# Performance work log

Hardware: AMD Instinct MI355X
Metric: run time of the kernel (lower is better)

## Reference

```python
import jax, jax.numpy as jnp
import numpy as np
import math


def setup_inputs() -> dict:
    rng = jax.random.key(0)
    k1, k2, k3 = jax.random.split(rng, 3)
    B, L, H, E = 2, 1024, 8, 64
    query = jax.random.normal(k1, (B, L, H, E), dtype=jnp.float32)
    key = jax.random.normal(k2, (B, L, H, E), dtype=jnp.float32)
    value = jax.random.normal(k3, (B, L, H, E), dtype=jnp.float32)
    mask_miss_k = jnp.zeros((B, L), dtype=bool)
    mask_miss_q = jnp.zeros((B, L), dtype=bool)
    pos = jnp.arange(B * L).reshape(B, L)
    causal_mask = 0  # unused by the module body
    # learned scalar parameters (nn.Parameter init values)
    log_gain_gate = jnp.float32(math.log(2.0))
    log_tau_gate = jnp.float32(math.log(0.5))
    log_gain_dir = jnp.float32(math.log(3.0))
    log_tau_dir = jnp.float32(math.log(0.3))
    return {
        "query": query, "key": key, "value": value,
        "mask_miss_k": mask_miss_k, "mask_miss_q": mask_miss_q,
        "pos": pos, "causal_mask": causal_mask,
        "log_gain_gate": log_gain_gate, "log_tau_gate": log_tau_gate,
        "log_gain_dir": log_gain_dir, "log_tau_dir": log_tau_dir,
    }


def reference(query, key, value, mask_miss_k, mask_miss_q, pos, causal_mask,
              log_gain_gate, log_tau_gate, log_gain_dir, log_tau_dir):
    # Multihead path: query (B,L,H,E). Eval mode, dropout p=0, dag_mask=None.
    B, L, H, E = query.shape
    scale = 1.0 / jnp.sqrt(jnp.float32(E))
    # scores: (B,H,L,S) with S == L
    scores = scale * jnp.einsum('blhe,bshe->bhls', query, key)
    scores_t = jnp.swapaxes(scores, -1, -2)
    S_sym = 0.5 * (scores + scores_t)       # symmetric part
    A_anti = 0.5 * (scores - scores_t)      # antisymmetric (Lie) part

    MAX_GAIN = 20.0
    gain_gate = jnp.clip(jnp.exp(log_gain_gate), 1e-3, MAX_GAIN)
    tau_gate = jnp.clip(jnp.exp(log_tau_gate), 1e-3, 10.0)
    gain_dir = jnp.clip(jnp.exp(log_gain_dir), 1e-3, MAX_GAIN)
    tau_dir = jnp.clip(jnp.exp(log_tau_dir), 1e-3, 10.0)

    gamma_att = gain_gate * jnp.tanh(S_sym / tau_gate)
    phi_att = gain_dir * jnp.tanh(A_anti / tau_dir)

    gate_probs = jax.nn.sigmoid(gamma_att)
    dir_probs = jax.nn.sigmoid(phi_att)
    dag_probs = gate_probs * dir_probs

    diag = jnp.eye(L, L, dtype=bool)  # P(i->i) = 0
    dag_probs = jnp.where(diag[None, None], 0.0, dag_probs)
    M = dag_probs  # eval branch; diagonal already zeroed (second fill is a no-op)

    att = jax.nn.relu(jnp.tanh(A_anti * gain_dir / tau_dir)) * M

    # entropy per query position (B,H,L)
    entropy = -jnp.sum(att * jnp.log(jnp.clip(att, 1e-8, None)), axis=-1)
    entropy = jnp.nan_to_num(entropy)

    # dropout p=0 -> identity; nan_to_num is a no-op on finite att
    V = jnp.einsum('bhls,bshd->blhd', att, value)  # (B,L,H,E)
    return V, att, entropy
```

## Files before the change

kernel.cpp:

```cpp
#include <hip/hip_runtime.h>
#include <math.h>

namespace {

typedef __bf16 bf16_t;
typedef bf16_t bf16x8 __attribute__((ext_vector_type(8)));
typedef bf16_t bf16x4 __attribute__((ext_vector_type(4)));
typedef bf16_t bf16x2 __attribute__((ext_vector_type(2)));
typedef float f32x4 __attribute__((ext_vector_type(4)));

constexpr int L = 1024;
constexpr int H = 8;
constexpr int E = 64;
constexpr int HE = H * E;
constexpr int BH = 16;
constexpr size_t PL = (size_t)BH * L * E;
constexpr float LOG2E = 1.4426950408889634f;
constexpr float LN2 = 0.6931471805599453f;

__device__ __forceinline__ float rcp_fast(float x) { return __builtin_amdgcn_rcpf(x); }
__device__ __forceinline__ float exp2_fast(float x) { return __builtin_amdgcn_exp2f(x); }
__device__ __forceinline__ float log2_fast(float x) { return __builtin_amdgcn_logf(x); }
__device__ __forceinline__ f32x4 mfma16(bf16x8 a, bf16x8 b, f32x4 c) {
  return __builtin_amdgcn_mfma_f32_16x16x32_bf16(a, b, c, 0, 0, 0);
}
__device__ __forceinline__ void split4(float4 x, bf16x4& hv, bf16x4& lv) {
  hv[0] = (bf16_t)x.x; lv[0] = (bf16_t)(x.x - (float)hv[0]);
  hv[1] = (bf16_t)x.y; lv[1] = (bf16_t)(x.y - (float)hv[1]);
  hv[2] = (bf16_t)x.z; lv[2] = (bf16_t)(x.z - (float)hv[2]);
  hv[3] = (bf16_t)x.w; lv[3] = (bf16_t)(x.w - (float)hv[3]);
}

__global__ __launch_bounds__(256) void k_prep(
    const float* __restrict__ q, const float* __restrict__ k,
    const float* __restrict__ v, bf16_t* __restrict__ ws,
    float* __restrict__ entr)
{
  const int bid = blockIdx.x;
  if (bid >= 256) {
    const int idx = (bid - 256) * 256 + threadIdx.x;
    *(float4*)(entr + (size_t)idx * 4) = make_float4(0.f, 0.f, 0.f, 0.f);
    return;
  }
  bf16_t* Qh = ws;
  bf16_t* Ql = ws + PL;
  bf16_t* Kh = ws + 2 * PL;
  bf16_t* Kl = ws + 3 * PL;
  bf16_t* VT = ws + 4 * PL;
  const int bh = bid >> 4, chunk = bid & 15;
  const int b = bh >> 3, h = bh & 7;
  const int tid = threadIdx.x, t8 = tid >> 4, c4 = tid & 15;
  __shared__ bf16_t Vb[64][72];

#pragma unroll
  for (int pass = 0; pass < 4; ++pass) {
    const int row = chunk * 64 + pass * 16 + t8;
    const size_t gin = ((size_t)(b * L + row) * H + h) * E + c4 * 4;
    const size_t gout = ((size_t)bh * L + row) * E + c4 * 4;
    float4 q4 = *(const float4*)(q + gin);
    float4 k4 = *(const float4*)(k + gin);
    float4 v4 = *(const float4*)(v + gin);
    bf16x4 hv, lv;
    split4(q4, hv, lv);
    *(bf16x4*)(Qh + gout) = hv; *(bf16x4*)(Ql + gout) = lv;
    split4(k4, hv, lv);
    *(bf16x4*)(Kh + gout) = hv; *(bf16x4*)(Kl + gout) = lv;
    const int sl = pass * 16 + t8;
    Vb[c4 * 4 + 0][sl] = (bf16_t)v4.x;
    Vb[c4 * 4 + 1][sl] = (bf16_t)v4.y;
    Vb[c4 * 4 + 2][sl] = (bf16_t)v4.z;
    Vb[c4 * 4 + 3][sl] = (bf16_t)v4.w;
  }
  __syncthreads();
#pragma unroll
  for (int pass = 0; pass < 2; ++pass) {
    const int idx = pass * 256 + tid;
    const int e = idx >> 3, ch = idx & 7;
    bf16x8 val = *(const bf16x8*)&Vb[e][ch * 8];
    *(bf16x8*)(VT + ((size_t)bh * E + e) * L + chunk * 64 + ch * 8) = val;
  }
}

__global__ __launch_bounds__(256, 2) void k_sym(
    const bf16_t* __restrict__ ws, float* __restrict__ attg,
    float* __restrict__ entr,
    const float* __restrict__ p_lgg, const float* __restrict__ p_ltg,
    const float* __restrict__ p_lgd, const float* __restrict__ p_ltd)
{
  const bf16_t* Qh = ws;
  const bf16_t* Ql = ws + PL;
  const bf16_t* Kh = ws + 2 * PL;
  const bf16_t* Kl = ws + 3 * PL;

  __shared__ __align__(16) bf16_t P_s[4][32][72];
  __shared__ __align__(16) float att2f[32][36];

  const int tid = threadIdx.x;
  const int w = tid >> 6, lane = tid & 63;
  const int c = lane & 15, qd = lane >> 4;
  const int lh = w & 1, sh = w >> 1;
  const int I = blockIdx.x, bh = blockIdx.y, z = blockIdx.z;
  const int niter = (I < 16) ? 17 : 16;
  const int itlo = z ? 8 : 0;
  const int ithi = z ? niter : 8;

  const float gg = fminf(fmaxf(__expf(p_lgg[0]), 1e-3f), 20.0f);
  const float tg = fminf(fmaxf(__expf(p_ltg[0]), 1e-3f), 10.0f);
  const float gd = fminf(fmaxf(__expf(p_lgd[0]), 1e-3f), 20.0f);
  const float td = fminf(fmaxf(__expf(p_ltd[0]), 1e-3f), 10.0f);
  const float A1 = 0.125f * (1.0f / tg) * LOG2E;
  const float A2 = 0.125f * (1.0f / td) * LOG2E;
  const float A3 = 0.125f * gd * (1.0f / td) * LOG2E;
  const float G1 = -gg * LOG2E, G1m2 = -2.0f * G1;
  const float G2 = -gd * LOG2E, G2m2 = -2.0f * G2;

  bf16x8 qaf[2][2], kaf[2][2];
  {
    const size_t aro = ((size_t)bh * L + I * 32 + lh * 16 + c) * E;
#pragma unroll
    for (int ks = 0; ks < 2; ++ks) {
      qaf[ks][0] = *(const bf16x8*)(Qh + aro + ks * 32 + qd * 8);
      qaf[ks][1] = *(const bf16x8*)(Ql + aro + ks * 32 + qd * 8);
      kaf[ks][0] = *(const bf16x8*)(Kh + aro + ks * 32 + qd * 8);
      kaf[ks][1] = *(const bf16x8*)(Kl + aro + ks * 32 + qd * 8);
    }
  }

  const bf16_t* planep = (w == 0) ? Kh : (w == 1) ? Kl : (w == 2) ? Qh : Ql;
  const int prow = lane >> 1;
  const int pcol = (lane & 1) * 32;

  bf16x8 pf0, pf1, pf2, pf3;
  {
    const size_t off =
        ((size_t)bh * L + (size_t)((I + itlo) & 31) * 32 + prow) * E + pcol;
    pf0 = *(const bf16x8*)(planep + off);
    pf1 = *(const bf16x8*)(planep + off + 8);
    pf2 = *(const bf16x8*)(planep + off + 16);
    pf3 = *(const bf16x8*)(planep + off + 24);
  }

  float entL[4] = {0.f, 0.f, 0.f, 0.f};

  for (int it = itlo; it < ithi; ++it) {
    const int J = (I + it) & 31;
    const int Jn = (I + it + 1) & 31;

    __syncthreads();
    *(bf16x8*)&P_s[w][prow][pcol]      = pf0;
    *(bf16x8*)&P_s[w][prow][pcol + 8]  = pf1;
    *(bf16x8*)&P_s[w][prow][pcol + 16] = pf2;
    *(bf16x8*)&P_s[w][prow][pcol + 24] = pf3;
    __syncthreads();

    {
      const size_t off = ((size_t)bh * L + (size_t)Jn * 32 + prow) * E + pcol;
      pf0 = *(const bf16x8*)(planep + off);
      pf1 = *(const bf16x8*)(planep + off + 8);
      pf2 = *(const bf16x8*)(planep + off + 16);
      pf3 = *(const bf16x8*)(planep + off + 24);
    }

    f32x4 acc1 = {}, acc2 = {};
    const int brow = sh * 16 + c;
#pragma unroll
    for (int ks = 0; ks < 2; ++ks) {
      bf16x8 kbh = *(const bf16x8*)&P_s[0][brow][ks * 32 + qd * 8];
      bf16x8 kbl = *(const bf16x8*)&P_s[1][brow][ks * 32 + qd * 8];
      bf16x8 qbh = *(const bf16x8*)&P_s[2][brow][ks * 32 + qd * 8];
      bf16x8 qbl = *(const bf16x8*)&P_s[3][brow][ks * 32 + qd * 8];
      acc1 = mfma16(qaf[ks][0], kbh, acc1);
      acc1 = mfma16(qaf[ks][0], kbl, acc1);
      acc1 = mfma16(qaf[ks][1], kbh, acc1);
      acc2 = mfma16(kaf[ks][0], qbh, acc2);
      acc2 = mfma16(kaf[ks][1], qbh, acc2);
      acc2 = mfma16(kaf[ks][0], qbl, acc2);
    }

    float entS = 0.f;
    float* arow = attg + ((size_t)bh * L + I * 32 + lh * 16 + qd * 4) * L +
                  (size_t)J * 32 + sh * 16;
    f32x4 a2v;
#pragma unroll
    for (int r = 0; r < 4; ++r) {
      const float u = acc1[r] + acc2[r];
      const float d = acc1[r] - acc2[r];
      const float r1 = rcp_fast(exp2_fast(u * A1) + 1.f);
      const float gate = rcp_fast(1.f + exp2_fast(fmaf(r1, G1m2, G1)));
      const float r2 = rcp_fast(exp2_fast(d * A2) + 1.f);
      const float dir = rcp_fast(1.f + exp2_fast(fmaf(r2, G2m2, G2)));
      const float t = fmaf(rcp_fast(exp2_fast(d * A3) + 1.f), -2.f, 1.f);
      const float gdp = gate * dir;
      const float a1 = fmaxf(t, 0.f) * gdp;
      const float a2 = fmaxf(-t, 0.f) * (gate - gdp);
      const float la = log2_fast(fmaxf(a1 + a2, 1e-8f));
      entL[r] -= a1 * la;
      entS -= a2 * la;
      arow[(size_t)r * L + c] = a1;
      a2v[r] = a2;
    }
    *(f32x4*)&att2f[sh * 16 + c][lh * 16 + qd * 4] = a2v;
    __syncthreads();

    if (it != 0) {
      const int mr = tid >> 3, mc = (tid & 7) * 4;
      float* orow =
          attg + ((size_t)bh * L + (size_t)J * 32 + mr) * L + (size_t)I * 32 + mc;
      *(f32x4*)orow = *(const f32x4*)&att2f[mr][mc];

      float e = entS;
      e += __shfl_xor(e, 16);
      e += __shfl_xor(e, 32);
      if (lane < 16)
        atomicAdd(entr + (size_t)bh * L + (size_t)J * 32 + sh * 16 + c, e * LN2);
    }
  }

#pragma unroll
  for (int r = 0; r < 4; ++r) {
    float e = entL[r];
    e += __shfl_xor(e, 1);
    e += __shfl_xor(e, 2);
    e += __shfl_xor(e, 4);
    e += __shfl_xor(e, 8);
    if (c == 0)
      atomicAdd(entr + (size_t)bh * L + I * 32 + lh * 16 + qd * 4 + r, e * LN2);
  }
}

__global__ __launch_bounds__(256, 2) void k_pv(
    const bf16_t* __restrict__ ws, const float* __restrict__ attg,
    float* __restrict__ Vout)
{
  const bf16_t* VT = ws + 4 * PL;
  __shared__ __align__(16) bf16_t att_s[32][72];

  const int tid = threadIdx.x;
  const int w = tid >> 6, lane = tid & 63;
  const int c = lane & 15, qd = lane >> 4;
  const int mh = w & 1, eh = w >> 1;
  const int lt = blockIdx.x, bh = blockIdx.y;
  const int b = bh >> 3, h = bh & 7;
  const int l0 = lt * 32;

  const int srow = tid >> 3, scol = (tid & 7) * 8;
  const float* abase = attg + ((size_t)bh * L + l0 + srow) * L + scol;

  f32x4 pa = *(const f32x4*)(abase);
  f32x4 pb = *(const f32x4*)(abase + 4);

  const bf16_t* vbase = VT + ((size_t)bh * E + eh * 32) * L;

  f32x4 acc[2] = {};
  for (int st = 0; st < 16; ++st) {
    __syncthreads();
    {
      bf16x8 af;
      af[0] = (bf16_t)pa[0]; af[1] = (bf16_t)pa[1];
      af[2] = (bf16_t)pa[2]; af[3] = (bf16_t)pa[3];
      af[4] = (bf16_t)pb[0]; af[5] = (bf16_t)pb[1];
      af[6] = (bf16_t)pb[2]; af[7] = (bf16_t)pb[3];
      *(bf16x8*)&att_s[srow][scol] = af;
    }
    __syncthreads();
    {
      const int stn = (st + 1) & 15;
      pa = *(const f32x4*)(abase + stn * 64);
      pb = *(const f32x4*)(abase + stn * 64 + 4);
    }
#pragma unroll
    for (int ks = 0; ks < 2; ++ks) {
      bf16x8 av = *(const bf16x8*)&att_s[mh * 16 + c][ks * 32 + qd * 8];
#pragma unroll
      for (int n = 0; n < 2; ++n) {
        bf16x8 bv = *(const bf16x8*)(vbase + (size_t)(n * 16 + c) * L +
                                     st * 64 + ks * 32 + qd * 8);
        acc[n] = mfma16(av, bv, acc[n]);
      }
    }
  }
#pragma unroll
  for (int n = 0; n < 2; ++n)
#pragma unroll
    for (int r = 0; r < 4; ++r)
      Vout[((size_t)(b * L + l0 + mh * 16 + qd * 4 + r) * H + h) * E +
           eh * 32 + n * 16 + c] = acc[n][r];
}

__device__ __forceinline__ float tanh_fast(float x) {
  return 1.0f - 2.0f * rcp_fast(__expf(2.0f * x) + 1.0f);
}
__device__ __forceinline__ float sigm_fast(float x) {
  return rcp_fast(1.0f + __expf(-x));
}
__device__ __forceinline__ void split_store(bf16_t* hi, bf16_t* lo, float4 x) {
  bf16x4 hv, lv;
  split4(x, hv, lv);
  *(bf16x4*)hi = hv;
  *(bf16x4*)lo = lv;
}

__global__ __launch_bounds__(128, 1) void fused_attn(
    const float* __restrict__ q, const float* __restrict__ kk,
    const float* __restrict__ v,
    float* __restrict__ Vout, float* __restrict__ attg, float* __restrict__ entr,
    const float* __restrict__ p_lgg, const float* __restrict__ p_ltg,
    const float* __restrict__ p_lgd, const float* __restrict__ p_ltd)
{
  constexpr int TM = 32;
  __shared__ bf16_t Qa_hi[TM][72], Qa_lo[TM][72];
  __shared__ bf16_t Ka_hi[TM][72], Ka_lo[TM][72];
  __shared__ bf16_t KQ_hi[64][72], KQ_lo[64][72];
  __shared__ bf16_t Vts[64][72];
  __shared__ float  T2ex[2][64][17];
  __shared__ bf16_t attLs[2][16][72];

  const int tid = threadIdx.x;
  const int w = tid >> 6;
  const int lane = tid & 63;
  const int c = lane & 15;
  const int qd = lane >> 4;
  const int t8 = tid >> 4;
  const int c4 = tid & 15;
  const int lt = blockIdx.x;
  const int bh = blockIdx.y;
  const int b = bh >> 3, h = bh & 7;
  const int l0 = lt * TM;

  const float gg = fminf(fmaxf(__expf(p_lgg[0]), 1e-3f), 20.0f);
  const float tg = fminf(fmaxf(__expf(p_ltg[0]), 1e-3f), 10.0f);
  const float gd = fminf(fmaxf(__expf(p_lgd[0]), 1e-3f), 20.0f);
  const float td = fminf(fmaxf(__expf(p_ltd[0]), 1e-3f), 10.0f);
  const float inv_tg = 1.0f / tg;
  const float inv_td = 1.0f / td;
  const float gd_inv_td = gd * inv_td;

  const float* qlbase = q  + ((size_t)(b * L + l0) * H + h) * E;
  const float* qsbase = q  + ((size_t)b * L * H + h) * E;
  const float* kbase  = kk + ((size_t)b * L * H + h) * E;
  const float* vbase  = v  + ((size_t)b * L * H + h) * E;

#pragma unroll
  for (int i = 0; i < 4; ++i) {
    int r = t8 + 8 * i;
    float4 qa = *(const float4*)(qlbase + (size_t)r * HE + c4 * 4);
    float4 ka = *(const float4*)(kbase + (size_t)(l0 + r) * HE + c4 * 4);
    split_store(&Qa_hi[r][c4 * 4], &Qa_lo[r][c4 * 4], qa);
    split_store(&Ka_hi[r][c4 * 4], &Ka_lo[r][c4 * 4], ka);
  }

  float4 kpre[8], qpre[8];
  float vpre[32];
#pragma unroll
  for (int i = 0; i < 8; ++i)
    kpre[i] = *(const float4*)(kbase + (size_t)(t8 + 8 * i) * HE + c4 * 4);
#pragma unroll
  for (int i = 0; i < 8; ++i)
    qpre[i] = *(const float4*)(qsbase + (size_t)(t8 + 8 * i) * HE + c4 * 4);
#pragma unroll
  for (int j = 0; j < 32; ++j)
    vpre[j] = vbase[(size_t)(w * 32 + j) * HE + lane];

  __syncthreads();

  bf16x8 qaf[2][2], kaf[2][2];
#pragma unroll
  for (int ks = 0; ks < 2; ++ks) {
    qaf[ks][0] = *(const bf16x8*)&Qa_hi[w * 16 + c][ks * 32 + qd * 8];
    qaf[ks][1] = *(const bf16x8*)&Qa_lo[w * 16 + c][ks * 32 + qd * 8];
    kaf[ks][0] = *(const bf16x8*)&Ka_hi[w * 16 + c][ks * 32 + qd * 8];
    kaf[ks][1] = *(const bf16x8*)&Ka_lo[w * 16 + c][ks * 32 + qd * 8];
  }

  f32x4 accv[4] = {};
  float ent[4] = {0.f, 0.f, 0.f, 0.f};
  const int gl_base = l0 + w * 16 + qd * 4;

  for (int it = 0; it < 16; ++it) {
    const int s0 = it * 64;
    const int snext = ((it + 1) & 15) * 64;

    __syncthreads();
#pragma unroll
    for (int i = 0; i < 8; ++i) {
      int r = t8 + 8 * i;
      split_store(&KQ_hi[r][c4 * 4], &KQ_lo[r][c4 * 4], kpre[i]);
    }
#pragma unroll
    for (int j = 0; j < 16; ++j) {
      bf16x2 p;
      p[0] = (bf16_t)vpre[2 * j];
      p[1] = (bf16_t)vpre[2 * j + 1];
      *(bf16x2*)&Vts[lane][w * 32 + 2 * j] = p;
    }
    __syncthreads();

#pragma unroll
    for (int i = 0; i < 8; ++i)
      kpre[i] = *(const float4*)(kbase + (size_t)(snext + t8 + 8 * i) * HE + c4 * 4);
#pragma unroll
    for (int j = 0; j < 32; ++j)
      vpre[j] = vbase[(size_t)(snext + w * 32 + j) * HE + lane];

    f32x4 acc1[4] = {};
#pragma unroll
    for (int nt = 0; nt < 4; ++nt) {
#pragma unroll
      for (int ks = 0; ks < 2; ++ks) {
        bf16x8 bhv = *(const bf16x8*)&KQ_hi[nt * 16 + c][ks * 32 + qd * 8];
        bf16x8 blv = *(const bf16x8*)&KQ_lo[nt * 16 + c][ks * 32 + qd * 8];
        acc1[nt] = mfma16(qaf[ks][0], bhv, acc1[nt]);
        acc1[nt] = mfma16(qaf[ks][0], blv, acc1[nt]);
        acc1[nt] = mfma16(qaf[ks][1], bhv, acc1[nt]);
      }
    }
    __syncthreads();

#pragma unroll
    for (int i = 0; i < 8; ++i) {
      int r = t8 + 8 * i;
      split_store(&KQ_hi[r][c4 * 4], &KQ_lo[r][c4 * 4], qpre[i]);
    }
    __syncthreads();

#pragma unroll
    for (int i = 0; i < 8; ++i)
      qpre[i] = *(const float4*)(qsbase + (size_t)(snext + t8 + 8 * i) * HE + c4 * 4);

    f32x4 acc2[4] = {};
#pragma unroll
    for (int mt = 0; mt < 4; ++mt) {
#pragma unroll
      for (int ks = 0; ks < 2; ++ks) {
        bf16x8 ahv = *(const bf16x8*)&KQ_hi[mt * 16 + c][ks * 32 + qd * 8];
        bf16x8 alv = *(const bf16x8*)&KQ_lo[mt * 16 + c][ks * 32 + qd * 8];
        acc2[mt] = mfma16(ahv, kaf[ks][0], acc2[mt]);
        acc2[mt] = mfma16(ahv, kaf[ks][1], acc2[mt]);
        acc2[mt] = mfma16(alv, kaf[ks][0], acc2[mt]);
      }
    }

#pragma unroll
    for (int mt = 0; mt < 4; ++mt)
#pragma unroll
      for (int r = 0; r < 4; ++r)
        T2ex[w][mt * 16 + qd * 4 + r][c] = acc2[mt][r];
    __syncthreads();

    float* attrow0 = attg + ((size_t)bh * L + gl_base) * L + s0;
#pragma unroll
    for (int nt = 0; nt < 4; ++nt) {
#pragma unroll
      for (int r = 0; r < 4; ++r) {
        float x = 0.125f * acc1[nt][r];
        float y = 0.125f * T2ex[w][nt * 16 + c][qd * 4 + r];
        float Ss = 0.5f * (x + y);
        float Aa = 0.5f * (x - y);
        float gate = sigm_fast(gg * tanh_fast(Ss * inv_tg));
        float dir  = sigm_fast(gd * tanh_fast(Aa * inv_td));
        float t    = tanh_fast(Aa * gd_inv_td);
        float a = fmaxf(t, 0.0f) * gate * dir;
        ent[r] -= a * __logf(fmaxf(a, 1e-8f));
        attrow0[(size_t)r * L + nt * 16 + c] = a;
        attLs[w][qd * 4 + r][nt * 16 + c] = (bf16_t)a;
      }
    }
    __syncthreads();

#pragma unroll
    for (int ks = 0; ks < 2; ++ks) {
      bf16x8 af = *(const bf16x8*)&attLs[w][c][ks * 32 + qd * 8];
#pragma unroll
      for (int ne = 0; ne < 4; ++ne) {
        bf16x8 bfv = *(const bf16x8*)&Vts[ne * 16 + c][ks * 32 + qd * 8];
        accv[ne] = mfma16(af, bfv, accv[ne]);
      }
    }
  }

#pragma unroll
  for (int r = 0; r < 4; ++r) {
    float* vb = Vout + ((size_t)(b * L + gl_base + r) * H + h) * E;
#pragma unroll
    for (int ne = 0; ne < 4; ++ne) vb[ne * 16 + c] = accv[ne][r];
    float e4 = ent[r];
    e4 += __shfl_xor(e4, 1);
    e4 += __shfl_xor(e4, 2);
    e4 += __shfl_xor(e4, 4);
    e4 += __shfl_xor(e4, 8);
    if (c == 0) entr[(size_t)bh * L + gl_base + r] = e4;
  }
}

}

extern "C" void kernel_launch(void* const* d_in, const int* in_sizes, int n_in,
                              void* d_out, int out_size, void* d_ws, size_t ws_size,
                              hipStream_t stream) {
  const float* q = (const float*)d_in[0];
  const float* k = (const float*)d_in[1];
  const float* v = (const float*)d_in[2];
  const float* p_lgg = (const float*)d_in[7];
  const float* p_ltg = (const float*)d_in[8];
  const float* p_lgd = (const float*)d_in[9];
  const float* p_ltd = (const float*)d_in[10];

  float* Vout = (float*)d_out;
  float* att  = Vout + 1048576;
  float* entr = att + 16777216;

  const size_t need = 5 * PL * sizeof(bf16_t);
  if (ws_size >= need) {
    bf16_t* ws = (bf16_t*)d_ws;
    k_prep<<<dim3(272), 256, 0, stream>>>(q, k, v, ws, entr);
    k_sym<<<dim3(32, 16, 2), 256, 0, stream>>>(
        ws, att, entr, p_lgg, p_ltg, p_lgd, p_ltd);
    k_pv<<<dim3(32, 16), 256, 0, stream>>>(ws, att, Vout);
  } else {
    fused_attn<<<dim3(32, 16), 128, 0, stream>>>(
        q, k, v, Vout, att, entr, p_lgg, p_ltg, p_lgd, p_ltd);
  }
}
```

Measured before the change: 151.8 us.

## Process paired key tiles in k_sym, drop LDS staging in k_pv, finer prep blocks

k_sym now handles two 32-column tiles per iteration over a 64-row shared stage. This halves the number of barrier and stage rounds, and the diagonal tile gets a cheaper path with no transpose write. k_pv drops its shared-memory staging and barriers, reading fp32 att straight from global into MFMA fragments, with occupancy hints raised. k_prep is split into twice as many smaller blocks. The price is more registers for the doubled prefetch and LDS footprint, plus uncoalesced direct loads in k_pv.

Result: slower. 168.3 us (+10.9%).

```diff
diff --git a/kernel.cpp b/kernel.cpp
--- a/kernel.cpp
+++ b/kernel.cpp
@@ -37,8 +37,8 @@
     float* __restrict__ entr)
 {
   const int bid = blockIdx.x;
-  if (bid >= 256) {
-    const int idx = (bid - 256) * 256 + threadIdx.x;
+  if (bid >= 512) {
+    const int idx = (bid - 512) * 256 + threadIdx.x;
     *(float4*)(entr + (size_t)idx * 4) = make_float4(0.f, 0.f, 0.f, 0.f);
     return;
   }
@@ -47,14 +47,14 @@
   bf16_t* Kh = ws + 2 * PL;
   bf16_t* Kl = ws + 3 * PL;
   bf16_t* VT = ws + 4 * PL;
-  const int bh = bid >> 4, chunk = bid & 15;
+  const int bh = bid >> 5, chunk = bid & 31;
   const int b = bh >> 3, h = bh & 7;
   const int tid = threadIdx.x, t8 = tid >> 4, c4 = tid & 15;
-  __shared__ bf16_t Vb[64][72];
-
-#pragma unroll
-  for (int pass = 0; pass < 4; ++pass) {
-    const int row = chunk * 64 + pass * 16 + t8;
+  __shared__ bf16_t Vb[64][40];
+
+#pragma unroll
+  for (int pass = 0; pass < 2; ++pass) {
+    const int row = chunk * 32 + pass * 16 + t8;
     const size_t gin = ((size_t)(b * L + row) * H + h) * E + c4 * 4;
     const size_t gout = ((size_t)bh * L + row) * E + c4 * 4;
     float4 q4 = *(const float4*)(q + gin);
@@ -72,16 +72,14 @@
     Vb[c4 * 4 + 3][sl] = (bf16_t)v4.w;
   }
   __syncthreads();
-#pragma unroll
-  for (int pass = 0; pass < 2; ++pass) {
-    const int idx = pass * 256 + tid;
-    const int e = idx >> 3, ch = idx & 7;
+  {
+    const int e = tid >> 2, ch = tid & 3;
     bf16x8 val = *(const bf16x8*)&Vb[e][ch * 8];
-    *(bf16x8*)(VT + ((size_t)bh * E + e) * L + chunk * 64 + ch * 8) = val;
-  }
-}
-
-__global__ __launch_bounds__(256, 2) void k_sym(
+    *(bf16x8*)(VT + ((size_t)bh * E + e) * L + chunk * 32 + ch * 8) = val;
+  }
+}
+
+__global__ __launch_bounds__(256, 3) void k_sym(
     const bf16_t* __restrict__ ws, float* __restrict__ attg,
     float* __restrict__ entr,
     const float* __restrict__ p_lgg, const float* __restrict__ p_ltg,
@@ -92,17 +90,32 @@
   const bf16_t* Kh = ws + 2 * PL;
   const bf16_t* Kl = ws + 3 * PL;
 
-  __shared__ __align__(16) bf16_t P_s[4][32][72];
-  __shared__ __align__(16) float att2f[32][36];
+  __shared__ __align__(16) bf16_t P_s[4][64][72];
+  __shared__ __align__(16) float att2f[2][32][36];
 
   const int tid = threadIdx.x;
   const int w = tid >> 6, lane = tid & 63;
   const int c = lane & 15, qd = lane >> 4;
   const int lh = w & 1, sh = w >> 1;
   const int I = blockIdx.x, bh = blockIdx.y, z = blockIdx.z;
-  const int niter = (I < 16) ? 17 : 16;
-  const int itlo = z ? 8 : 0;
-  const int ithi = z ? niter : 8;
+  const int ghi = (I < 16) ? 16 : 15;
+  const int nu = z ? 4 : 5;
+
+  auto unitJ = [&](int u, int& J0, int& J1, bool& t1, bool& dg) {
+    if (z == 0) {
+      if (u == 0) { J0 = I; J1 = I; t1 = false; dg = true; }
+      else {
+        const int g = 2 * u - 1;
+        J0 = (I + g) & 31; J1 = (I + g + 1) & 31; t1 = true; dg = false;
+      }
+    } else {
+      const int g = 9 + 2 * u;
+      J0 = (I + g) & 31;
+      t1 = (g + 1) <= ghi;
+      J1 = t1 ? ((I + g + 1) & 31) : J0;
+      dg = false;
+    }
+  };
 
   const float gg = fminf(fmaxf(__expf(p_lgg[0]), 1e-3f), 20.0f);
   const float tg = fminf(fmaxf(__expf(p_ltg[0]), 1e-3f), 10.0f);
@@ -127,92 +140,129 @@
   }
 
   const bf16_t* planep = (w == 0) ? Kh : (w == 1) ? Kl : (w == 2) ? Qh : Ql;
-  const int prow = lane >> 1;
-  const int pcol = (lane & 1) * 32;
-
-  bf16x8 pf0, pf1, pf2, pf3;
+  const int lrow = lane & 31;
+  const int lsel = lane >> 5;
+
+  bf16x8 pf[8];
   {
-    const size_t off =
-        ((size_t)bh * L + (size_t)((I + itlo) & 31) * 32 + prow) * E + pcol;
-    pf0 = *(const bf16x8*)(planep + off);
-    pf1 = *(const bf16x8*)(planep + off + 8);
-    pf2 = *(const bf16x8*)(planep + off + 16);
-    pf3 = *(const bf16x8*)(planep + off + 24);
+    int J0, J1; bool t1, dg;
+    unitJ(0, J0, J1, t1, dg);
+    const size_t off = ((size_t)bh * L + (size_t)(lsel ? J1 : J0) * 32 + lrow) * E;
+#pragma unroll
+    for (int j = 0; j < 8; ++j) pf[j] = *(const bf16x8*)(planep + off + j * 8);
   }
 
   float entL[4] = {0.f, 0.f, 0.f, 0.f};
 
-  for (int it = itlo; it < ithi; ++it) {
-    const int J = (I + it) & 31;
-    const int Jn = (I + it + 1) & 31;
-
-    __syncthreads();
-    *(bf16x8*)&P_s[w][prow][pcol]      = pf0;
-    *(bf16x8*)&P_s[w][prow][pcol + 8]  = pf1;
-    *(bf16x8*)&P_s[w][prow][pcol + 16] = pf2;
-    *(bf16x8*)&P_s[w][prow][pcol + 24] = pf3;
+  for (int u = 0; u < nu; ++u) {
+    int J0, J1; bool t1v, dflag;
+    unitJ(u, J0, J1, t1v, dflag);
+    const int ntile = t1v ? 2 : 1;
+    const int Jv[2] = {J0, J1};
+
+    __syncthreads();
+#pragma unroll
+    for (int j = 0; j < 8; ++j) *(bf16x8*)&P_s[w][lane][j * 8] = pf[j];
     __syncthreads();
 
     {
-      const size_t off = ((size_t)bh * L + (size_t)Jn * 32 + prow) * E + pcol;
-      pf0 = *(const bf16x8*)(planep + off);
-      pf1 = *(const bf16x8*)(planep + off + 8);
-      pf2 = *(const bf16x8*)(planep + off + 16);
-      pf3 = *(const bf16x8*)(planep + off + 24);
-    }
-
-    f32x4 acc1 = {}, acc2 = {};
-    const int brow = sh * 16 + c;
-#pragma unroll
-    for (int ks = 0; ks < 2; ++ks) {
-      bf16x8 kbh = *(const bf16x8*)&P_s[0][brow][ks * 32 + qd * 8];
-      bf16x8 kbl = *(const bf16x8*)&P_s[1][brow][ks * 32 + qd * 8];
-      bf16x8 qbh = *(const bf16x8*)&P_s[2][brow][ks * 32 + qd * 8];
-      bf16x8 qbl = *(const bf16x8*)&P_s[3][brow][ks * 32 + qd * 8];
-      acc1 = mfma16(qaf[ks][0], kbh, acc1);
-      acc1 = mfma16(qaf[ks][0], kbl, acc1);
-      acc1 = mfma16(qaf[ks][1], kbh, acc1);
-      acc2 = mfma16(kaf[ks][0], qbh, acc2);
-      acc2 = mfma16(kaf[ks][1], qbh, acc2);
-      acc2 = mfma16(kaf[ks][0], qbl, acc2);
-    }
-
-    float entS = 0.f;
-    float* arow = attg + ((size_t)bh * L + I * 32 + lh * 16 + qd * 4) * L +
-                  (size_t)J * 32 + sh * 16;
-    f32x4 a2v;
-#pragma unroll
-    for (int r = 0; r < 4; ++r) {
-      const float u = acc1[r] + acc2[r];
-      const float d = acc1[r] - acc2[r];
-      const float r1 = rcp_fast(exp2_fast(u * A1) + 1.f);
-      const float gate = rcp_fast(1.f + exp2_fast(fmaf(r1, G1m2, G1)));
-      const float r2 = rcp_fast(exp2_fast(d * A2) + 1.f);
-      const float dir = rcp_fast(1.f + exp2_fast(fmaf(r2, G2m2, G2)));
-      const float t = fmaf(rcp_fast(exp2_fast(d * A3) + 1.f), -2.f, 1.f);
-      const float gdp = gate * dir;
-      const float a1 = fmaxf(t, 0.f) * gdp;
-      const float a2 = fmaxf(-t, 0.f) * (gate - gdp);
-      const float la = log2_fast(fmaxf(a1 + a2, 1e-8f));
-      entL[r] -= a1 * la;
-      entS -= a2 * la;
-      arow[(size_t)r * L + c] = a1;
-      a2v[r] = a2;
-    }
-    *(f32x4*)&att2f[sh * 16 + c][lh * 16 + qd * 4] = a2v;
-    __syncthreads();
-
-    if (it != 0) {
+      int nJ0, nJ1; bool nt1, ndg;
+      unitJ(u + 1, nJ0, nJ1, nt1, ndg);
+      const size_t off =
+          ((size_t)bh * L + (size_t)(lsel ? nJ1 : nJ0) * 32 + lrow) * E;
+#pragma unroll
+      for (int j = 0; j < 8; ++j) pf[j] = *(const bf16x8*)(planep + off + j * 8);
+    }
+
+    f32x4 acc1[2] = {}, acc2[2] = {};
+#pragma unroll
+    for (int t = 0; t < 2; ++t) {
+      if (t < ntile) {
+        const int brow = t * 32 + sh * 16 + c;
+#pragma unroll
+        for (int ks = 0; ks < 2; ++ks) {
+          bf16x8 kbh = *(const bf16x8*)&P_s[0][brow][ks * 32 + qd * 8];
+          bf16x8 kbl = *(const bf16x8*)&P_s[1][brow][ks * 32 + qd * 8];
+          bf16x8 qbh = *(const bf16x8*)&P_s[2][brow][ks * 32 + qd * 8];
+          bf16x8 qbl = *(const bf16x8*)&P_s[3][brow][ks * 32 + qd * 8];
+          acc1[t] = mfma16(qaf[ks][0], kbh, acc1[t]);
+          acc1[t] = mfma16(qaf[ks][0], kbl, acc1[t]);
+          acc1[t] = mfma16(qaf[ks][1], kbh, acc1[t]);
+          acc2[t] = mfma16(kaf[ks][0], qbh, acc2[t]);
+          acc2[t] = mfma16(kaf[ks][1], qbh, acc2[t]);
+          acc2[t] = mfma16(kaf[ks][0], qbl, acc2[t]);
+        }
+      }
+    }
+
+    float entS[2] = {0.f, 0.f};
+#pragma unroll
+    for (int t = 0; t < 2; ++t) {
+      if (t < ntile) {
+        float* arow = attg + ((size_t)bh * L + I * 32 + lh * 16 + qd * 4) * L +
+                      (size_t)Jv[t] * 32 + sh * 16;
+        if (!dflag) {
+          f32x4 a2v;
+#pragma unroll
+          for (int r = 0; r < 4; ++r) {
+            const float u_ = acc1[t][r] + acc2[t][r];
+            const float d_ = acc1[t][r] - acc2[t][r];
+            const float r1 = rcp_fast(exp2_fast(u_ * A1) + 1.f);
+            const float gate = rcp_fast(1.f + exp2_fast(fmaf(r1, G1m2, G1)));
+            const float r2 = rcp_fast(exp2_fast(d_ * A2) + 1.f);
+            const float dir = rcp_fast(1.f + exp2_fast(fmaf(r2, G2m2, G2)));
+            const float tt = fmaf(rcp_fast(exp2_fast(d_ * A3) + 1.f), -2.f, 1.f);
+            const float gdp = gate * dir;
+            const float a1 = fmaxf(tt, 0.f) * gdp;
+            const float a2 = fmaxf(-tt, 0.f) * (gate - gdp);
+            const float la = log2_fast(fmaxf(a1 + a2, 1e-8f));
+            entL[r] -= a1 * la;
+            entS[t] -= a2 * la;
+            arow[(size_t)r * L + c] = a1;
+            a2v[r] = a2;
+          }
+          *(f32x4*)&att2f[t][sh * 16 + c][lh * 16 + qd * 4] = a2v;
+        } else {
+#pragma unroll
+          for (int r = 0; r < 4; ++r) {
+            const float u_ = acc1[t][r] + acc2[t][r];
+            const float d_ = acc1[t][r] - acc2[t][r];
+            const float r1 = rcp_fast(exp2_fast(u_ * A1) + 1.f);
+            const float gate = rcp_fast(1.f + exp2_fast(fmaf(r1, G1m2, G1)));
+            const float r2 = rcp_fast(exp2_fast(d_ * A2) + 1.f);
+            const float dir = rcp_fast(1.f + exp2_fast(fmaf(r2, G2m2, G2)));
+            const float tt = fmaf(rcp_fast(exp2_fast(d_ * A3) + 1.f), -2.f, 1.f);
+            const float a1 = fmaxf(tt, 0.f) * gate * dir;
+            const float la = log2_fast(fmaxf(a1, 1e-8f));
+            entL[r] -= a1 * la;
+            arow[(size_t)r * L + c] = a1;
+          }
+        }
+      }
+    }
+    __syncthreads();
+
+    if (!dflag) {
       const int mr = tid >> 3, mc = (tid & 7) * 4;
-      float* orow =
-          attg + ((size_t)bh * L + (size_t)J * 32 + mr) * L + (size_t)I * 32 + mc;
-      *(f32x4*)orow = *(const f32x4*)&att2f[mr][mc];
-
-      float e = entS;
-      e += __shfl_xor(e, 16);
-      e += __shfl_xor(e, 32);
-      if (lane < 16)
-        atomicAdd(entr + (size_t)bh * L + (size_t)J * 32 + sh * 16 + c, e * LN2);
+#pragma unroll
+      for (int t = 0; t < 2; ++t) {
+        if (t < ntile) {
+          float* orow = attg + ((size_t)bh * L + (size_t)Jv[t] * 32 + mr) * L +
+                        (size_t)I * 32 + mc;
+          *(f32x4*)orow = *(const f32x4*)&att2f[t][mr][mc];
+        }
+      }
+#pragma unroll
+      for (int t = 0; t < 2; ++t) {
+        if (t < ntile) {
+          float e = entS[t];
+          e += __shfl_xor(e, 16);
+          e += __shfl_xor(e, 32);
+          if (lane < 16)
+            atomicAdd(entr + (size_t)bh * L + (size_t)Jv[t] * 32 + sh * 16 + c,
+                      e * LN2);
+        }
+      }
     }
   }
 
@@ -228,62 +278,46 @@
   }
 }
 
-__global__ __launch_bounds__(256, 2) void k_pv(
+__global__ __launch_bounds__(256, 4) void k_pv(
     const bf16_t* __restrict__ ws, const float* __restrict__ attg,
     float* __restrict__ Vout)
 {
   const bf16_t* VT = ws + 4 * PL;
-  __shared__ __align__(16) bf16_t att_s[32][72];
-
   const int tid = threadIdx.x;
   const int w = tid >> 6, lane = tid & 63;
   const int c = lane & 15, qd = lane >> 4;
   const int mh = w & 1, eh = w >> 1;
   const int lt = blockIdx.x, bh = blockIdx.y;
   const int b = bh >> 3, h = bh & 7;
-  const int l0 = lt * 32;
-
-  const int srow = tid >> 3, scol = (tid & 7) * 8;
-  const float* abase = attg + ((size_t)bh * L + l0 + srow) * L + scol;
-
-  f32x4 pa = *(const f32x4*)(abase);
-  f32x4 pb = *(const f32x4*)(abase + 4);
-
-  const bf16_t* vbase = VT + ((size_t)bh * E + eh * 32) * L;
+  const int l0 = lt * 32 + mh * 16;
+
+  const float* arow = attg + ((size_t)bh * L + l0 + c) * L + qd * 8;
+  const bf16_t* vrow = VT + ((size_t)bh * E + eh * 32 + c) * L + qd * 8;
 
   f32x4 acc[2] = {};
+#pragma unroll 4
   for (int st = 0; st < 16; ++st) {
-    __syncthreads();
-    {
-      bf16x8 af;
-      af[0] = (bf16_t)pa[0]; af[1] = (bf16_t)pa[1];
-      af[2] = (bf16_t)pa[2]; af[3] = (bf16_t)pa[3];
-      af[4] = (bf16_t)pb[0]; af[5] = (bf16_t)pb[1];
-      af[6] = (bf16_t)pb[2]; af[7] = (bf16_t)pb[3];
-      *(bf16x8*)&att_s[srow][scol] = af;
-    }
-    __syncthreads();
-    {
-      const int stn = (st + 1) & 15;
-      pa = *(const f32x4*)(abase + stn * 64);
-      pb = *(const f32x4*)(abase + stn * 64 + 4);
-    }
 #pragma unroll
     for (int ks = 0; ks < 2; ++ks) {
-      bf16x8 av = *(const bf16x8*)&att_s[mh * 16 + c][ks * 32 + qd * 8];
-#pragma unroll
-      for (int n = 0; n < 2; ++n) {
-        bf16x8 bv = *(const bf16x8*)(vbase + (size_t)(n * 16 + c) * L +
-                                     st * 64 + ks * 32 + qd * 8);
-        acc[n] = mfma16(av, bv, acc[n]);
-      }
+      const int off = st * 64 + ks * 32;
+      f32x4 a0 = *(const f32x4*)(arow + off);
+      f32x4 a1 = *(const f32x4*)(arow + off + 4);
+      bf16x8 av;
+      av[0] = (bf16_t)a0[0]; av[1] = (bf16_t)a0[1];
+      av[2] = (bf16_t)a0[2]; av[3] = (bf16_t)a0[3];
+      av[4] = (bf16_t)a1[0]; av[5] = (bf16_t)a1[1];
+      av[6] = (bf16_t)a1[2]; av[7] = (bf16_t)a1[3];
+      bf16x8 b0 = *(const bf16x8*)(vrow + off);
+      bf16x8 b1 = *(const bf16x8*)(vrow + (size_t)16 * L + off);
+      acc[0] = mfma16(av, b0, acc[0]);
+      acc[1] = mfma16(av, b1, acc[1]);
     }
   }
 #pragma unroll
   for (int n = 0; n < 2; ++n)
 #pragma unroll
     for (int r = 0; r < 4; ++r)
-      Vout[((size_t)(b * L + l0 + mh * 16 + qd * 4 + r) * H + h) * E +
+      Vout[((size_t)(b * L + l0 + qd * 4 + r) * H + h) * E +
            eh * 32 + n * 16 + c] = acc[n][r];
 }
 
@@ -512,7 +546,7 @@
   const size_t need = 5 * PL * sizeof(bf16_t);
   if (ws_size >= need) {
     bf16_t* ws = (bf16_t*)d_ws;
-    k_prep<<<dim3(272), 256, 0, stream>>>(q, k, v, ws, entr);
+    k_prep<<<dim3(528), 256, 0, stream>>>(q, k, v, ws, entr);
     k_sym<<<dim3(32, 16, 2), 256, 0, stream>>>(
         ws, att, entr, p_lgg, p_ltg, p_lgd, p_ltd);
     k_pv<<<dim3(32, 16), 256, 0, stream>>>(ws, att, Vout);
```
